# Kernel optimization log

Hardware: AMD Instinct MI355X
Metric: run time of the kernel (lower is better)

The kernel has to match this reference:

```python
import jax, jax.numpy as jnp
import numpy as np

B, N, EM = 16, 1024, 768
D_K, D_V, H = 768, 768, 12

def setup_inputs() -> dict:
    key = jax.random.key(0)
    ks = jax.random.split(key, 4)
    s = 0.02
    x = jax.random.normal(ks[0], (B, N, EM), dtype=jnp.float32)
    W_qk = jax.random.normal(ks[1], (EM, 2 * D_K), dtype=jnp.float32) * s
    b_qk = jnp.zeros((2 * D_K,), dtype=jnp.float32)
    W_v = jax.random.normal(ks[2], (EM, D_V), dtype=jnp.float32) * s
    b_v = jnp.zeros((D_V,), dtype=jnp.float32)
    W_proj = jax.random.normal(ks[3], (D_V, EM), dtype=jnp.float32) * s
    b_proj = jnp.zeros((EM,), dtype=jnp.float32)
    return {"x": x, "W_qk": W_qk, "b_qk": b_qk, "W_v": W_v, "b_v": b_v,
            "W_proj": W_proj, "b_proj": b_proj}

def reference(x, W_qk, b_qk, W_v, b_v, W_proj, b_proj):
    b, n, _ = x.shape
    d = D_K // H  # per-head dim
    # qk Linear -> [B,N,2*d_K]; rearrange 'b n (h d qk) -> qk b h n d'
    # i.e. last dim splits as (h, d, 2) with qk fastest-varying.
    qk = (x @ W_qk + b_qk).reshape(b, n, H, d, 2)
    Q = jnp.transpose(qk[..., 0], (0, 2, 1, 3))  # [B,H,N,d]
    K = jnp.transpose(qk[..., 1], (0, 2, 1, 3))  # [B,H,N,d]
    V = (x @ W_v + b_v).reshape(b, n, H, D_V // H).transpose(0, 2, 1, 3)  # [B,H,N,dv]
    scores = jnp.einsum('bhqd,bhkd->bhqk', Q, K) / jnp.sqrt(jnp.float32(d))
    att = jax.nn.softmax(scores, axis=-1)  # dropout p=0 -> identity
    out = jnp.einsum('bhqk,bhkv->bhqv', att, V)  # [B,H,N,dv]
    out = out.transpose(0, 2, 1, 3).reshape(b, n, D_V)
    return out @ W_proj + b_proj
```

## Files before the change

### kernel.cpp

```cpp
#include <hip/hip_runtime.h>
#include <hip/hip_bf16.h>
#include <stdint.h>

typedef unsigned short u16;
typedef __bf16 bf16_t;
typedef bf16_t bf16x8 __attribute__((ext_vector_type(8)));
typedef short s16x4 __attribute__((ext_vector_type(4)));
typedef float f32x4 __attribute__((ext_vector_type(4)));

__device__ __forceinline__ u16 f2bf(float f) {
    union { float f; uint32_t i; } v; v.f = f;
    uint32_t i = v.i;
    uint32_t r = (i + 0x7FFFu + ((i >> 16) & 1u)) >> 16;
    return (u16)r;
}

__device__ __forceinline__ void gload_lds16(const u16* g, u16* l) {
    auto gp = (const __attribute__((address_space(1))) void*)g;
    auto lp = (__attribute__((address_space(3))) void*)(uintptr_t)l;
    __builtin_amdgcn_global_load_lds(gp, lp, 16, 0, 0);
}

__global__ void convert_f32_bf16_kernel(const float* __restrict__ src,
                                        u16* __restrict__ dst, int n4) {
    int i = blockIdx.x * blockDim.x + threadIdx.x;
    if (i < n4) {
        float4 v = ((const float4*)src)[i];
        ushort4 o;
        o.x = f2bf(v.x); o.y = f2bf(v.y); o.z = f2bf(v.z); o.w = f2bf(v.w);
        ((ushort4*)dst)[i] = o;
    }
}

__global__ void transpose_qk_kernel(const float* __restrict__ W, const float* __restrict__ b,
                                    u16* __restrict__ Wt, float* __restrict__ bp) {
    int r = blockIdx.x;
    int qk = (r >= 768) ? 1 : 0;
    int hd = r - qk * 768;
    int c = (hd >> 6) * 128 + (hd & 63) * 2 + qk;
    float s = qk ? 1.0f : 0.125f;
    for (int k = threadIdx.x; k < 768; k += 256)
        Wt[r * 768 + k] = f2bf(s * W[k * 1536 + c]);
    if (threadIdx.x == 0) bp[r] = s * b[c];
}

__global__ void transpose_sq_kernel(const float* __restrict__ W, u16* __restrict__ Wt) {
    int n = blockIdx.x;
    for (int k = threadIdx.x; k < 768; k += 256)
        Wt[n * 768 + k] = f2bf(W[k * 768 + n]);
}

template<int MODE>
__global__ __launch_bounds__(256)
void gemm_bt_kernel(const u16* __restrict__ A, const u16* __restrict__ Bt,
                    const float* __restrict__ bias, void* __restrict__ Cout,
                    void* __restrict__ Cout2, int M, int N, int K) {
    __shared__ __attribute__((aligned(16))) u16 As[128 * 32];
    __shared__ __attribute__((aligned(16))) u16 Bs[128 * 32];

    const int tid  = threadIdx.x;
    const int lane = tid & 63;
    const int wave = tid >> 6;
    const int l16  = lane & 15;
    const int quad = lane >> 4;
    const int m0 = blockIdx.y * 128;
    const int n0 = blockIdx.x * 128;
    const int wm = (wave & 1) * 64;
    const int wn = (wave >> 1) * 64;

    f32x4 acc[4][4];
#pragma unroll
    for (int i = 0; i < 4; i++)
#pragma unroll
        for (int j = 0; j < 4; j++) acc[i][j] = (f32x4){0.f, 0.f, 0.f, 0.f};

    const int rs = lane >> 2;
    const int sA = (lane & 3) ^ ((lane >> 3) & 3);
    const u16* Ag0 = A  + (size_t)(m0 + wave * 32 + rs) * K + sA * 8;
    const u16* Ag1 = Ag0 + (size_t)16 * K;
    const u16* Bg0 = Bt + (size_t)(n0 + wave * 32 + rs) * K + sA * 8;
    const u16* Bg1 = Bg0 + (size_t)16 * K;
    u16* AsW = As + wave * 1024;
    u16* BsW = Bs + wave * 1024;
    const int swq = (l16 >> 1) & 3;

    for (int k0 = 0; k0 < K; k0 += 32) {
        gload_lds16(Ag0 + k0, AsW);
        gload_lds16(Ag1 + k0, AsW + 512);
        gload_lds16(Bg0 + k0, BsW);
        gload_lds16(Bg1 + k0, BsW + 512);
        __syncthreads();

        bf16x8 af[4], bfr[4];
#pragma unroll
        for (int i = 0; i < 4; i++) {
            af[i]  = *(const bf16x8*)&As[(wm + i * 16 + l16) * 32 + ((quad ^ swq) * 8)];
            bfr[i] = *(const bf16x8*)&Bs[(wn + i * 16 + l16) * 32 + ((quad ^ swq) * 8)];
        }
#pragma unroll
        for (int i = 0; i < 4; i++)
#pragma unroll
            for (int j = 0; j < 4; j++) {
                if constexpr (MODE == 3)
                    acc[i][j] = __builtin_amdgcn_mfma_f32_16x16x32_bf16(af[i], bfr[j], acc[i][j], 0, 0, 0);
                else
                    acc[i][j] = __builtin_amdgcn_mfma_f32_16x16x32_bf16(bfr[j], af[i], acc[i][j], 0, 0, 0);
            }
        __syncthreads();
    }

    if constexpr (MODE == 3) {
#pragma unroll
        for (int j = 0; j < 4; j++) {
            int cnb = n0 + wn + j * 16;
            int h   = cnb >> 6;
            int dv  = (cnb & 63) + l16;
            float bv = bias[cnb + l16];
#pragma unroll
            for (int i = 0; i < 4; i++) {
                int cm = m0 + wm + i * 16 + quad * 4;
                int bb = cm >> 10, n = cm & 1023;
                ushort4 o;
                o.x = f2bf(acc[i][j][0] + bv);
                o.y = f2bf(acc[i][j][1] + bv);
                o.z = f2bf(acc[i][j][2] + bv);
                o.w = f2bf(acc[i][j][3] + bv);
                *(ushort4*)&((u16*)Cout)[((size_t)((bb * 12 + h) * 64 + dv)) * 1024 + n] = o;
            }
        }
    } else {
#pragma unroll
        for (int j = 0; j < 4; j++) {
            int f0 = n0 + wn + j * 16 + quad * 4;
            float4 bv = *(const float4*)&bias[f0];
            if constexpr (MODE == 2) {
                int qk = f0 >= 768;
                int hd = f0 - qk * 768;
                int h  = hd >> 6;
                int d0 = hd & 63;
                u16* dst = (u16*)(qk ? Cout2 : Cout);
#pragma unroll
                for (int i = 0; i < 4; i++) {
                    int t = m0 + wm + i * 16 + l16;
                    int bb = t >> 10, n = t & 1023;
                    ushort4 o;
                    o.x = f2bf(acc[i][j][0] + bv.x);
                    o.y = f2bf(acc[i][j][1] + bv.y);
                    o.z = f2bf(acc[i][j][2] + bv.z);
                    o.w = f2bf(acc[i][j][3] + bv.w);
                    *(ushort4*)&dst[((size_t)((bb * 12 + h) * 1024 + n)) * 64 + d0] = o;
                }
            } else {
#pragma unroll
                for (int i = 0; i < 4; i++) {
                    int t = m0 + wm + i * 16 + l16;
                    float4 o;
                    o.x = acc[i][j][0] + bv.x;
                    o.y = acc[i][j][1] + bv.y;
                    o.z = acc[i][j][2] + bv.z;
                    o.w = acc[i][j][3] + bv.w;
                    *(float4*)&((float*)Cout)[(size_t)t * N + f0] = o;
                }
            }
        }
    }
}

__global__ __launch_bounds__(512)
void attention_mfma_kernel(const u16* __restrict__ Qp, const u16* __restrict__ Kp,
                           const u16* __restrict__ Vp, u16* __restrict__ attout) {
    __shared__ __attribute__((aligned(16))) u16 Ks[64 * 64];
    __shared__ __attribute__((aligned(16))) u16 Vs[64 * 64];

    const int tid  = threadIdx.x;
    const int wave = tid >> 6;
    const int lane = tid & 63;
    const int l16  = lane & 15;
    const int quad = lane >> 4;
    const int bh = blockIdx.y;
    const int b  = bh / 12, h = bh % 12;
    const int q0 = blockIdx.x * 256 + wave * 32;

    const u16* Qhead = Qp + (size_t)bh * 1024 * 64;
    const u16* Khead = Kp + (size_t)bh * 1024 * 64;
    const u16* Vhead = Vp + (size_t)bh * 64 * 1024;

    bf16x8 qf[2][2];
#pragma unroll
    for (int qb = 0; qb < 2; qb++) {
        const u16* qrow = Qhead + (size_t)(q0 + qb * 16 + l16) * 64;
        qf[qb][0] = *(const bf16x8*)(qrow + quad * 8);
        qf[qb][1] = *(const bf16x8*)(qrow + 32 + quad * 8);
    }

    f32x4 oacc[2][4];
#pragma unroll
    for (int qb = 0; qb < 2; qb++)
#pragma unroll
        for (int db = 0; db < 4; db++) oacc[qb][db] = (f32x4){0.f, 0.f, 0.f, 0.f};
    float l_part[2] = {0.f, 0.f};

    const int srow = tid >> 3;
    const int gseg = (tid & 7) ^ (srow & 7);
    u16* KsW = Ks + wave * 512;
    u16* VsW = Vs + wave * 512;
    const int sw7 = l16 & 7;

    for (int kt = 0; kt < 1024; kt += 64) {
        gload_lds16(Khead + (size_t)(kt + srow) * 64 + gseg * 8, KsW);
        gload_lds16(Vhead + (size_t)srow * 1024 + kt + gseg * 8, VsW);
        __syncthreads();

        s16x4 pf[2][4];
        {
            bf16x8 kf[4][2];
#pragma unroll
            for (int jb = 0; jb < 4; jb++) {
#pragma unroll
                for (int hf = 0; hf < 2; hf++)
                    kf[jb][hf] = *(const bf16x8*)&Ks[(jb * 16 + l16) * 64 +
                                                     (((hf * 4 + quad) ^ sw7) * 8)];
            }
#pragma unroll
            for (int qb = 0; qb < 2; qb++) {
#pragma unroll
                for (int jb = 0; jb < 4; jb++) {
                    f32x4 st = (f32x4){0.f, 0.f, 0.f, 0.f};
                    st = __builtin_amdgcn_mfma_f32_16x16x32_bf16(kf[jb][0], qf[qb][0], st, 0, 0, 0);
                    st = __builtin_amdgcn_mfma_f32_16x16x32_bf16(kf[jb][1], qf[qb][1], st, 0, 0, 0);
                    float e0 = __expf(st[0]), e1 = __expf(st[1]);
                    float e2 = __expf(st[2]), e3 = __expf(st[3]);
                    l_part[qb] += (e0 + e1) + (e2 + e3);
                    union { __hip_bfloat162 h2; uint32_t u; } c0, c1;
                    c0.h2 = __float22bfloat162_rn(make_float2(e0, e1));
                    c1.h2 = __float22bfloat162_rn(make_float2(e2, e3));
                    union { uint32_t u2[2]; s16x4 v; } pk;
                    pk.u2[0] = c0.u; pk.u2[1] = c1.u;
                    pf[qb][jb] = pk.v;
                }
            }
        }

#pragma unroll
        for (int db = 0; db < 4; db++) {
            s16x4 vb[4];
#pragma unroll
            for (int jb = 0; jb < 4; jb++) {
                int g = jb * 2 + (quad >> 1);
                vb[jb] = *(const s16x4*)&Vs[(db * 16 + l16) * 64 +
                                            ((g ^ sw7) * 8) + (quad & 1) * 4];
            }
#pragma unroll
            for (int qb = 0; qb < 2; qb++)
#pragma unroll
                for (int jb = 0; jb < 4; jb++)
                    oacc[qb][db] = __builtin_amdgcn_mfma_f32_16x16x16bf16_1k(
                        pf[qb][jb], vb[jb], oacc[qb][db], 0, 0, 0);
        }
        __syncthreads();
    }

#pragma unroll
    for (int qb = 0; qb < 2; qb++) {
        float l = l_part[qb];
        l += __shfl_xor(l, 16);
        l += __shfl_xor(l, 32);
        float linv[4];
#pragma unroll
        for (int r = 0; r < 4; r++)
            linv[r] = 1.0f / __shfl(l, quad * 4 + r);
        u16* orow = attout + (size_t)(b * 1024 + q0 + qb * 16 + quad * 4) * 768 + h * 64 + l16;
#pragma unroll
        for (int db = 0; db < 4; db++)
#pragma unroll
            for (int r = 0; r < 4; r++)
                orow[(size_t)r * 768 + db * 16] = f2bf(oacc[qb][db][r] * linv[r]);
    }
}

extern "C" void kernel_launch(void* const* d_in, const int* in_sizes, int n_in,
                              void* d_out, int out_size, void* d_ws, size_t ws_size,
                              hipStream_t stream) {
    const float* x      = (const float*)d_in[0];
    const float* W_qk   = (const float*)d_in[1];
    const float* b_qk   = (const float*)d_in[2];
    const float* W_v    = (const float*)d_in[3];
    const float* b_v    = (const float*)d_in[4];
    const float* W_proj = (const float*)d_in[5];
    const float* b_proj = (const float*)d_in[6];
    float* out = (float*)d_out;

    char* ws = (char*)d_ws;
    size_t off = 0;
    auto alloc = [&](size_t bytes) { void* p = ws + off; off += (bytes + 255) & ~255ull; return p; };
    u16*   xb     = (u16*)alloc((size_t)16384 * 768 * 2);
    u16*   Wqkt   = (u16*)alloc((size_t)1536 * 768 * 2);
    float* bqkp   = (float*)alloc(1536 * 4);
    u16*   Wvt    = (u16*)alloc((size_t)768 * 768 * 2);
    u16*   Wprojt = (u16*)alloc((size_t)768 * 768 * 2);
    u16*   Qp     = (u16*)alloc((size_t)16384 * 768 * 2);
    u16*   Kp     = (u16*)alloc((size_t)16384 * 768 * 2);
    u16*   Vp     = (u16*)alloc((size_t)16384 * 768 * 2);
    u16*   attout = (u16*)alloc((size_t)16384 * 768 * 2);

    convert_f32_bf16_kernel<<<12288, 256, 0, stream>>>(x, xb, 3145728);
    transpose_qk_kernel<<<1536, 256, 0, stream>>>(W_qk, b_qk, Wqkt, bqkp);
    transpose_sq_kernel<<<768, 256, 0, stream>>>(W_v, Wvt);
    transpose_sq_kernel<<<768, 256, 0, stream>>>(W_proj, Wprojt);

    gemm_bt_kernel<2><<<dim3(12, 128), 256, 0, stream>>>(xb, Wqkt, bqkp, Qp, Kp, 16384, 1536, 768);
    gemm_bt_kernel<3><<<dim3(6, 128), 256, 0, stream>>>(xb, Wvt, b_v, Vp, nullptr, 16384, 768, 768);
    attention_mfma_kernel<<<dim3(4, 192), 512, 0, stream>>>(Qp, Kp, Vp, attout);
    gemm_bt_kernel<1><<<dim3(6, 128), 256, 0, stream>>>(attout, Wprojt, b_proj, out, nullptr, 16384, 768, 768);
}
```

Baseline: 355.0 us.

## Double GEMM K-tile to 64 and use 16x16x32 MFMA for PV

The projection GEMM now stages 64-wide K slices per iteration, with an 8-way XOR swizzle and four 16-byte async loads per operand. This halves the number of barrier-separated iterations and doubles the MFMA work between syncs. In attention, the P·V product now packs pairs of key blocks into bf16x8 operands and issues 16x16x32 MFMAs instead of 16x16x16, halving the MFMA instruction count. The cost is doubled LDS use in the GEMM, which may reduce occupancy, and more register pressure.

```diff
diff --git a/kernel.cpp b/kernel.cpp
--- a/kernel.cpp
+++ b/kernel.cpp
@@ -55,8 +55,8 @@
 void gemm_bt_kernel(const u16* __restrict__ A, const u16* __restrict__ Bt,
                     const float* __restrict__ bias, void* __restrict__ Cout,
                     void* __restrict__ Cout2, int M, int N, int K) {
-    __shared__ __attribute__((aligned(16))) u16 As[128 * 32];
-    __shared__ __attribute__((aligned(16))) u16 Bs[128 * 32];
+    __shared__ __attribute__((aligned(16))) u16 As[128 * 64];
+    __shared__ __attribute__((aligned(16))) u16 Bs[128 * 64];
 
     const int tid  = threadIdx.x;
     const int lane = tid & 63;
@@ -74,37 +74,48 @@
 #pragma unroll
         for (int j = 0; j < 4; j++) acc[i][j] = (f32x4){0.f, 0.f, 0.f, 0.f};
 
-    const int rs = lane >> 2;
-    const int sA = (lane & 3) ^ ((lane >> 3) & 3);
-    const u16* Ag0 = A  + (size_t)(m0 + wave * 32 + rs) * K + sA * 8;
-    const u16* Ag1 = Ag0 + (size_t)16 * K;
-    const u16* Bg0 = Bt + (size_t)(n0 + wave * 32 + rs) * K + sA * 8;
-    const u16* Bg1 = Bg0 + (size_t)16 * K;
-    u16* AsW = As + wave * 1024;
-    u16* BsW = Bs + wave * 1024;
-    const int swq = (l16 >> 1) & 3;
-
-    for (int k0 = 0; k0 < K; k0 += 32) {
-        gload_lds16(Ag0 + k0, AsW);
-        gload_lds16(Ag1 + k0, AsW + 512);
-        gload_lds16(Bg0 + k0, BsW);
-        gload_lds16(Bg1 + k0, BsW + 512);
+    const int rs   = lane >> 3;
+    const int gseg = (lane & 7) ^ rs;
+    const u16* Ag[4]; const u16* Bg[4];
+#pragma unroll
+    for (int c = 0; c < 4; c++) {
+        Ag[c] = A  + (size_t)(m0 + c * 32 + wave * 8 + rs) * K + gseg * 8;
+        Bg[c] = Bt + (size_t)(n0 + c * 32 + wave * 8 + rs) * K + gseg * 8;
+    }
+    u16* AsW = As + wave * 512;
+    u16* BsW = Bs + wave * 512;
+    const int sw7 = l16 & 7;
+
+    for (int k0 = 0; k0 < K; k0 += 64) {
+#pragma unroll
+        for (int c = 0; c < 4; c++) {
+            gload_lds16(Ag[c] + k0, AsW + c * 2048);
+            gload_lds16(Bg[c] + k0, BsW + c * 2048);
+        }
         __syncthreads();
 
-        bf16x8 af[4], bfr[4];
+        bf16x8 af[4][2], bfr[4][2];
 #pragma unroll
         for (int i = 0; i < 4; i++) {
-            af[i]  = *(const bf16x8*)&As[(wm + i * 16 + l16) * 32 + ((quad ^ swq) * 8)];
-            bfr[i] = *(const bf16x8*)&Bs[(wn + i * 16 + l16) * 32 + ((quad ^ swq) * 8)];
+#pragma unroll
+            for (int h = 0; h < 2; h++) {
+                af[i][h]  = *(const bf16x8*)&As[(wm + i * 16 + l16) * 64 +
+                                                (((h * 4 + quad) ^ sw7) * 8)];
+                bfr[i][h] = *(const bf16x8*)&Bs[(wn + i * 16 + l16) * 64 +
+                                                (((h * 4 + quad) ^ sw7) * 8)];
+            }
         }
 #pragma unroll
         for (int i = 0; i < 4; i++)
 #pragma unroll
             for (int j = 0; j < 4; j++) {
-                if constexpr (MODE == 3)
-                    acc[i][j] = __builtin_amdgcn_mfma_f32_16x16x32_bf16(af[i], bfr[j], acc[i][j], 0, 0, 0);
-                else
-                    acc[i][j] = __builtin_amdgcn_mfma_f32_16x16x32_bf16(bfr[j], af[i], acc[i][j], 0, 0, 0);
+#pragma unroll
+                for (int h = 0; h < 2; h++) {
+                    if constexpr (MODE == 3)
+                        acc[i][j] = __builtin_amdgcn_mfma_f32_16x16x32_bf16(af[i][h], bfr[j][h], acc[i][j], 0, 0, 0);
+                    else
+                        acc[i][j] = __builtin_amdgcn_mfma_f32_16x16x32_bf16(bfr[j][h], af[i][h], acc[i][j], 0, 0, 0);
+                }
             }
         __syncthreads();
     }
@@ -211,7 +222,7 @@
         gload_lds16(Vhead + (size_t)srow * 1024 + kt + gseg * 8, VsW);
         __syncthreads();
 
-        s16x4 pf[2][4];
+        union { uint32_t u[4]; bf16x8 v; } pf8[2][2];
         {
             bf16x8 kf[4][2];
 #pragma unroll
@@ -234,28 +245,28 @@
                     union { __hip_bfloat162 h2; uint32_t u; } c0, c1;
                     c0.h2 = __float22bfloat162_rn(make_float2(e0, e1));
                     c1.h2 = __float22bfloat162_rn(make_float2(e2, e3));
-                    union { uint32_t u2[2]; s16x4 v; } pk;
-                    pk.u2[0] = c0.u; pk.u2[1] = c1.u;
-                    pf[qb][jb] = pk.v;
+                    pf8[qb][jb >> 1].u[(jb & 1) * 2 + 0] = c0.u;
+                    pf8[qb][jb >> 1].u[(jb & 1) * 2 + 1] = c1.u;
                 }
             }
         }
 
 #pragma unroll
         for (int db = 0; db < 4; db++) {
-            s16x4 vb[4];
-#pragma unroll
-            for (int jb = 0; jb < 4; jb++) {
-                int g = jb * 2 + (quad >> 1);
-                vb[jb] = *(const s16x4*)&Vs[(db * 16 + l16) * 64 +
-                                            ((g ^ sw7) * 8) + (quad & 1) * 4];
-            }
-#pragma unroll
-            for (int qb = 0; qb < 2; qb++)
-#pragma unroll
-                for (int jb = 0; jb < 4; jb++)
-                    oacc[qb][db] = __builtin_amdgcn_mfma_f32_16x16x16bf16_1k(
-                        pf[qb][jb], vb[jb], oacc[qb][db], 0, 0, 0);
+#pragma unroll
+            for (int jp = 0; jp < 2; jp++) {
+                union { s16x4 h[2]; bf16x8 v; } vb8;
+                int glo = 4 * jp + (quad >> 1);
+                int ghi = glo + 2;
+                vb8.h[0] = *(const s16x4*)&Vs[(db * 16 + l16) * 64 +
+                                              ((glo ^ sw7) * 8) + (quad & 1) * 4];
+                vb8.h[1] = *(const s16x4*)&Vs[(db * 16 + l16) * 64 +
+                                              ((ghi ^ sw7) * 8) + (quad & 1) * 4];
+#pragma unroll
+                for (int qb = 0; qb < 2; qb++)
+                    oacc[qb][db] = __builtin_amdgcn_mfma_f32_16x16x32_bf16(
+                        pf8[qb][jp].v, vb8.v, oacc[qb][db], 0, 0, 0);
+            }
         }
         __syncthreads();
     }
```

Measured after the change: 345.0 us. 1.03x faster.
